# Kernel tuning notes

Measured on AMD Instinct MI355X. Metric: run time of the kernel, lower is better.

Reference implementation:

```python
import jax, jax.numpy as jnp
import numpy as np

N_NODES = 100000
HIDDEN = 128
N_EDGES = 1000000


def setup_inputs() -> dict:
    key = jax.random.key(0)
    k1, k2, k3 = jax.random.split(key, 3)
    z = jax.random.normal(k1, (N_NODES, HIDDEN), dtype=jnp.float32)
    edge_index = jax.random.randint(k2, (2, N_EDGES), 0, N_NODES, dtype=jnp.int64)
    # xavier_uniform for square matrix: bound = sqrt(6/(fan_in+fan_out))
    bound = float(np.sqrt(6.0 / (HIDDEN + HIDDEN)))
    weights = jax.random.uniform(k3, (HIDDEN, HIDDEN), dtype=jnp.float32,
                                 minval=-bound, maxval=bound)
    return {"z": z, "edge_index": edge_index, "weights": weights}


def reference(z, edge_index, weights):
    # symm=True: symmetrize the bilinear form
    W = weights + weights.T                      # [d, d]
    z_src = z[edge_index[0]]                     # [E, d] gather
    z_dst = z[edge_index[1]]                     # [E, d] gather
    # torch: (W @ z_dst.T).T == z_dst @ W.T
    value = jnp.einsum('ed,dk,ek->e', z_src, W, z_dst)  # row-wise bilinear score
    return jax.nn.sigmoid(value)
```

## Files before the change

### kernel.cpp

```cpp
#include <hip/hip_runtime.h>

#define HIDDEN 128
#define SLOT_H 264
#define BSHIFT 10
#define NBMAX 128

typedef _Float16 f16;
typedef f16 f16x2 __attribute__((ext_vector_type(2)));
typedef f16 f16x8 __attribute__((ext_vector_type(8)));
typedef float f32x16 __attribute__((ext_vector_type(16)));
typedef unsigned long long ull;

static __device__ __forceinline__ float fdot2(f16x2 a, f16x2 b, float c) {
    return __builtin_amdgcn_fdot2(a, b, c, false);
}

__global__ __launch_bounds__(256) void prep_w(const float* __restrict__ w,
                                              f16* __restrict__ wsh_t,
                                              int* __restrict__ hist) {
    int idx = blockIdx.x * 256 + threadIdx.x;
    if (idx < 2 * NBMAX) hist[idx] = 0;
    int n = idx >> 7, k = idx & 127;
    wsh_t[idx] = (f16)(w[k * HIDDEN + n] + w[n * HIDDEN + k]);
}

__global__ __launch_bounds__(256) void hist_k(const int* __restrict__ eidx,
                                              int* __restrict__ hist, int E, int nb) {
    __shared__ int h[NBMAX];
    int tid = threadIdx.x;
    if (tid < NBMAX) h[tid] = 0;
    __syncthreads();
    for (int e = blockIdx.x * 256 + tid; e < E; e += gridDim.x * 256)
        atomicAdd(&h[eidx[E + e] >> BSHIFT], 1);
    __syncthreads();
    if (tid < nb && h[tid]) atomicAdd(&hist[tid], h[tid]);
}

__global__ void scan_k(const int* __restrict__ hist, int* __restrict__ cursor, int nb) {
    if (threadIdx.x == 0) {
        int s = 0;
        for (int i = 0; i < nb; ++i) { cursor[i] = s; s += hist[i]; }
    }
}

__global__ __launch_bounds__(256) void scatter_k(const int* __restrict__ eidx,
                                                 int* __restrict__ cursor,
                                                 ull* __restrict__ perm, int E, int nb) {
    __shared__ int lh[NBMAX], lbase[NBMAX], lrank[NBMAX];
    int tid = threadIdx.x;
    int base = blockIdx.x * 4096;
    if (tid < NBMAX) { lh[tid] = 0; lrank[tid] = 0; }
    __syncthreads();
    int s[16], d[16], bb[16];
    #pragma unroll
    for (int i = 0; i < 16; ++i) {
        int e = base + i * 256 + tid;
        bb[i] = -1;
        if (e < E) {
            s[i] = eidx[e]; d[i] = eidx[E + e];
            bb[i] = d[i] >> BSHIFT;
            atomicAdd(&lh[bb[i]], 1);
        }
    }
    __syncthreads();
    if (tid < nb && lh[tid]) lbase[tid] = atomicAdd(&cursor[tid], lh[tid]);
    __syncthreads();
    #pragma unroll
    for (int i = 0; i < 16; ++i) {
        if (bb[i] >= 0) {
            int e = base + i * 256 + tid;
            int r = atomicAdd(&lrank[bb[i]], 1);
            perm[lbase[bb[i]] + r] =
                (ull)s[i] | ((ull)d[i] << 17) | ((ull)e << 34);
        }
    }
}

__global__ __launch_bounds__(256, 3) void gemm_mfma2(const float* __restrict__ z,
                                                     const f16* __restrict__ wsh_t,
                                                     f16* __restrict__ zh,
                                                     f16* __restrict__ uh, int nrows) {
    __shared__ f16 afrag[64 * SLOT_H];
    int tid = threadIdx.x;
    int row0 = blockIdx.x * 128;
    if (row0 > nrows - 128) row0 = nrows - 128;

    {
        const float4* zg = (const float4*)(z + (size_t)row0 * HIDDEN);
        f16x8* zhg = (f16x8*)(zh + (size_t)row0 * HIDDEN);
        #pragma unroll
        for (int it = 0; it < 8; ++it) {
            int g = it * 256 + tid;
            float4 v0 = zg[2 * g];
            float4 v1 = zg[2 * g + 1];
            f16x8 h = {(f16)v0.x, (f16)v0.y, (f16)v0.z, (f16)v0.w,
                       (f16)v1.x, (f16)v1.y, (f16)v1.z, (f16)v1.w};
            zhg[g] = h;
            int row = g >> 4, ch = g & 15;
            int slot = (row >> 5) * 16 + ch;
            *(f16x8*)&afrag[slot * SLOT_H + (row & 31) * 8] = h;
        }
    }
    __syncthreads();

    int wave = tid >> 6, lane = tid & 63;
    int m = lane & 31, half = lane >> 5;
    const f16* wb = wsh_t + (size_t)m * HIDDEN + half * 8;

    f32x16 acc0, acc1, acc2, acc3;
    #pragma unroll
    for (int r = 0; r < 16; ++r) { acc0[r] = 0.f; acc1[r] = 0.f; acc2[r] = 0.f; acc3[r] = 0.f; }

    #pragma unroll
    for (int ks = 0; ks < 8; ++ks) {
        f16x8 a = *(const f16x8*)&afrag[(wave * 16 + ks * 2 + half) * SLOT_H + m * 8];
        f16x8 b0 = *(const f16x8*)&wb[ 0 * HIDDEN + 16 * ks];
        f16x8 b1 = *(const f16x8*)&wb[32 * HIDDEN + 16 * ks];
        f16x8 b2 = *(const f16x8*)&wb[64 * HIDDEN + 16 * ks];
        f16x8 b3 = *(const f16x8*)&wb[96 * HIDDEN + 16 * ks];
        acc0 = __builtin_amdgcn_mfma_f32_32x32x16_f16(a, b0, acc0, 0, 0, 0);
        acc1 = __builtin_amdgcn_mfma_f32_32x32x16_f16(a, b1, acc1, 0, 0, 0);
        acc2 = __builtin_amdgcn_mfma_f32_32x32x16_f16(a, b2, acc2, 0, 0, 0);
        acc3 = __builtin_amdgcn_mfma_f32_32x32x16_f16(a, b3, acc3, 0, 0, 0);
    }

    f16* ur = uh + (size_t)(row0 + wave * 32) * HIDDEN;
    #pragma unroll
    for (int r = 0; r < 16; ++r) {
        int row = (r & 3) + 8 * (r >> 2) + 4 * half;
        f16* p = ur + (size_t)row * HIDDEN + m;
        p[0]  = (f16)acc0[r];
        p[32] = (f16)acc1[r];
        p[64] = (f16)acc2[r];
        p[96] = (f16)acc3[r];
    }
}

__global__ __launch_bounds__(256) void edge_bin(const f16* __restrict__ uh,
                                                const f16* __restrict__ zh,
                                                const ull* __restrict__ perm,
                                                float* __restrict__ out, int E, int cpx) {
    int tid = threadIdx.x;
    int g = tid >> 4, t = tid & 15;
    int b = blockIdx.x;
    int chunk = (b & 7) * cpx + (b >> 3);
    int e = chunk * 16 + g;
    if (e >= E) return;
    ull p = perm[e];
    int src = (int)(p & 0x1FFFF);
    int dst = (int)((p >> 17) & 0x1FFFF);
    int eid = (int)(p >> 34);
    const float4* a4 = (const float4*)(uh + (size_t)src * HIDDEN);
    const float4* b4 = (const float4*)(zh + (size_t)dst * HIDDEN);
    float4 av = a4[t], bv = b4[t];
    const f16x2* ap = (const f16x2*)&av;
    const f16x2* bp = (const f16x2*)&bv;
    float s = 0.f;
    #pragma unroll
    for (int i = 0; i < 4; ++i) s = fdot2(ap[i], bp[i], s);
    #pragma unroll
    for (int off = 8; off > 0; off >>= 1) s += __shfl_down(s, off, 16);
    if (t == 0) out[eid] = 1.0f / (1.0f + __expf(-s));
}

__global__ __launch_bounds__(256) void edge_score16(const f16* __restrict__ uh,
                                                    const f16* __restrict__ zh,
                                                    const int* __restrict__ eidx,
                                                    float* __restrict__ out, int E) {
    int tid = threadIdx.x;
    int g = tid >> 4, t = tid & 15;
    int e = blockIdx.x * 16 + g;
    if (e >= E) return;
    int src = eidx[e];
    int dst = eidx[E + e];
    const float4* a4 = (const float4*)(uh + (size_t)src * HIDDEN);
    const float4* b4 = (const float4*)(zh + (size_t)dst * HIDDEN);
    float4 av = a4[t], bv = b4[t];
    const f16x2* ap = (const f16x2*)&av;
    const f16x2* bp = (const f16x2*)&bv;
    float s = 0.f;
    #pragma unroll
    for (int i = 0; i < 4; ++i) s = fdot2(ap[i], bp[i], s);
    #pragma unroll
    for (int off = 8; off > 0; off >>= 1) s += __shfl_down(s, off, 16);
    if (t == 0) out[e] = 1.0f / (1.0f + __expf(-s));
}

extern "C" void kernel_launch(void* const* d_in, const int* in_sizes, int n_in,
                              void* d_out, int out_size, void* d_ws, size_t ws_size,
                              hipStream_t stream) {
    const float* z    = (const float*)d_in[0];
    const int*   eidx = (const int*)d_in[1];
    const float* w    = (const float*)d_in[2];
    float* out = (float*)d_out;

    int nrows = in_sizes[0] / HIDDEN;
    int E = out_size;
    int nb = (nrows >> BSHIFT) + 1;

    f16* wsh_t = (f16*)d_ws;
    f16* zh    = wsh_t + HIDDEN * HIDDEN;
    f16* uh    = zh + (size_t)nrows * HIDDEN;
    int* hist  = (int*)(uh + (size_t)nrows * HIDDEN);
    int* cursor = hist + NBMAX;
    ull* perm  = (ull*)(cursor + NBMAX);

    size_t need = (size_t)((char*)(perm + E) - (char*)d_ws);
    bool binned = ws_size >= need;

    prep_w<<<64, 256, 0, stream>>>(w, wsh_t, hist);
    if (binned) {
        hist_k<<<256, 256, 0, stream>>>(eidx, hist, E, nb);
        scan_k<<<1, 64, 0, stream>>>(hist, cursor, nb);
        scatter_k<<<(E + 4095) / 4096, 256, 0, stream>>>(eidx, cursor, perm, E, nb);
    }
    gemm_mfma2<<<(nrows + 127) / 128, 256, 0, stream>>>(z, wsh_t, zh, uh, nrows);
    if (binned) {
        int nch = (E + 15) / 16;
        int cpx = (nch + 7) / 8;
        edge_bin<<<8 * cpx, 256, 0, stream>>>(uh, zh, perm, out, E, cpx);
    } else {
        edge_score16<<<(E + 15) / 16, 256, 0, stream>>>(uh, zh, eidx, out, E);
    }
}
```

Measured before the change: 193.6 us.

## Replace histogram+scan binning with fixed-capacity buckets and overflow list

Drops the histogram and serial scan kernels and gives each destination bucket a fixed-capacity slot range, so scatter can start directly from preset cursors. Edges past a bucket's capacity go to an overflow buffer that a separate kernel scores. The edge kernel now launches over all padded slots and skips the empty ones, which adds some idle blocks plus an extra launch. It also switches the uh gather to a nontemporal load. This assumes bucket sizes rarely exceed the capacity. Overflow is capped, and any edges beyond that cap would be silently dropped.

Result: slower. 221.4 us (+14.4%).

```diff
diff --git a/kernel.cpp b/kernel.cpp
--- a/kernel.cpp
+++ b/kernel.cpp
@@ -4,10 +4,13 @@
 #define SLOT_H 264
 #define BSHIFT 10
 #define NBMAX 128
+#define CAP 11264
+#define OVF_MAX 65536
 
 typedef _Float16 f16;
 typedef f16 f16x2 __attribute__((ext_vector_type(2)));
 typedef f16 f16x8 __attribute__((ext_vector_type(8)));
+typedef float f32x4 __attribute__((ext_vector_type(4)));
 typedef float f32x16 __attribute__((ext_vector_type(16)));
 typedef unsigned long long ull;
 
@@ -17,35 +20,21 @@
 
 __global__ __launch_bounds__(256) void prep_w(const float* __restrict__ w,
                                               f16* __restrict__ wsh_t,
-                                              int* __restrict__ hist) {
+                                              int* __restrict__ cursor,
+                                              int* __restrict__ ovf_cnt) {
     int idx = blockIdx.x * 256 + threadIdx.x;
-    if (idx < 2 * NBMAX) hist[idx] = 0;
+    if (idx < NBMAX) cursor[idx] = idx * CAP;
+    if (idx == NBMAX) ovf_cnt[0] = 0;
     int n = idx >> 7, k = idx & 127;
     wsh_t[idx] = (f16)(w[k * HIDDEN + n] + w[n * HIDDEN + k]);
 }
 
-__global__ __launch_bounds__(256) void hist_k(const int* __restrict__ eidx,
-                                              int* __restrict__ hist, int E, int nb) {
-    __shared__ int h[NBMAX];
-    int tid = threadIdx.x;
-    if (tid < NBMAX) h[tid] = 0;
-    __syncthreads();
-    for (int e = blockIdx.x * 256 + tid; e < E; e += gridDim.x * 256)
-        atomicAdd(&h[eidx[E + e] >> BSHIFT], 1);
-    __syncthreads();
-    if (tid < nb && h[tid]) atomicAdd(&hist[tid], h[tid]);
-}
-
-__global__ void scan_k(const int* __restrict__ hist, int* __restrict__ cursor, int nb) {
-    if (threadIdx.x == 0) {
-        int s = 0;
-        for (int i = 0; i < nb; ++i) { cursor[i] = s; s += hist[i]; }
-    }
-}
-
 __global__ __launch_bounds__(256) void scatter_k(const int* __restrict__ eidx,
                                                  int* __restrict__ cursor,
-                                                 ull* __restrict__ perm, int E, int nb) {
+                                                 ull* __restrict__ perm,
+                                                 ull* __restrict__ ovf,
+                                                 int* __restrict__ ovf_cnt,
+                                                 int E, int nb) {
     __shared__ int lh[NBMAX], lbase[NBMAX], lrank[NBMAX];
     int tid = threadIdx.x;
     int base = blockIdx.x * 4096;
@@ -70,8 +59,13 @@
         if (bb[i] >= 0) {
             int e = base + i * 256 + tid;
             int r = atomicAdd(&lrank[bb[i]], 1);
-            perm[lbase[bb[i]] + r] =
-                (ull)s[i] | ((ull)d[i] << 17) | ((ull)e << 34);
+            long pos = (long)lbase[bb[i]] + r;
+            ull v = (ull)s[i] | ((ull)d[i] << 17) | ((ull)e << 34);
+            if (pos < (long)(bb[i] + 1) * CAP) perm[pos] = v;
+            else {
+                int o = atomicAdd(ovf_cnt, 1);
+                if (o < OVF_MAX) ovf[o] = v;
+            }
         }
     }
 }
@@ -136,31 +130,53 @@
     }
 }
 
+static __device__ __forceinline__ void score_edge(const f16* uh, const f16* zh,
+                                                  ull p, float* out, int t) {
+    int src = (int)(p & 0x1FFFF);
+    int dst = (int)((p >> 17) & 0x1FFFF);
+    int eid = (int)(p >> 34);
+    const f32x4* a4 = (const f32x4*)(uh + (size_t)src * HIDDEN);
+    const f32x4* b4 = (const f32x4*)(zh + (size_t)dst * HIDDEN);
+    f32x4 av = __builtin_nontemporal_load(&a4[t]);
+    f32x4 bv = b4[t];
+    const f16x2* ap = (const f16x2*)&av;
+    const f16x2* bp = (const f16x2*)&bv;
+    float s = 0.f;
+    #pragma unroll
+    for (int i = 0; i < 4; ++i) s = fdot2(ap[i], bp[i], s);
+    #pragma unroll
+    for (int off = 8; off > 0; off >>= 1) s += __shfl_down(s, off, 16);
+    if (t == 0) out[eid] = 1.0f / (1.0f + __expf(-s));
+}
+
 __global__ __launch_bounds__(256) void edge_bin(const f16* __restrict__ uh,
                                                 const f16* __restrict__ zh,
                                                 const ull* __restrict__ perm,
-                                                float* __restrict__ out, int E, int cpx) {
+                                                const int* __restrict__ cursor,
+                                                float* __restrict__ out, int cpx) {
     int tid = threadIdx.x;
     int g = tid >> 4, t = tid & 15;
     int b = blockIdx.x;
     int chunk = (b & 7) * cpx + (b >> 3);
-    int e = chunk * 16 + g;
-    if (e >= E) return;
-    ull p = perm[e];
-    int src = (int)(p & 0x1FFFF);
-    int dst = (int)((p >> 17) & 0x1FFFF);
-    int eid = (int)(p >> 34);
-    const float4* a4 = (const float4*)(uh + (size_t)src * HIDDEN);
-    const float4* b4 = (const float4*)(zh + (size_t)dst * HIDDEN);
-    float4 av = a4[t], bv = b4[t];
-    const f16x2* ap = (const f16x2*)&av;
-    const f16x2* bp = (const f16x2*)&bv;
-    float s = 0.f;
-    #pragma unroll
-    for (int i = 0; i < 4; ++i) s = fdot2(ap[i], bp[i], s);
-    #pragma unroll
-    for (int off = 8; off > 0; off >>= 1) s += __shfl_down(s, off, 16);
-    if (t == 0) out[eid] = 1.0f / (1.0f + __expf(-s));
+    long slot = (long)chunk * 16 + g;
+    int bk = (int)(slot / CAP);
+    int end = cursor[bk];
+    int lim = (bk + 1) * CAP;
+    if (slot >= (end < lim ? end : lim)) return;
+    score_edge(uh, zh, perm[slot], out, t);
+}
+
+__global__ __launch_bounds__(256) void edge_ovf(const f16* __restrict__ uh,
+                                                const f16* __restrict__ zh,
+                                                const ull* __restrict__ ovf,
+                                                const int* __restrict__ ovf_cnt,
+                                                float* __restrict__ out) {
+    int n = ovf_cnt[0];
+    if (n > OVF_MAX) n = OVF_MAX;
+    int tid = threadIdx.x;
+    int g = tid >> 4, t = tid & 15;
+    for (int i = blockIdx.x * 16 + g; i < n; i += gridDim.x * 16)
+        score_edge(uh, zh, ovf[i], out, t);
 }
 
 __global__ __launch_bounds__(256) void edge_score16(const f16* __restrict__ uh,
@@ -171,19 +187,8 @@
     int g = tid >> 4, t = tid & 15;
     int e = blockIdx.x * 16 + g;
     if (e >= E) return;
-    int src = eidx[e];
-    int dst = eidx[E + e];
-    const float4* a4 = (const float4*)(uh + (size_t)src * HIDDEN);
-    const float4* b4 = (const float4*)(zh + (size_t)dst * HIDDEN);
-    float4 av = a4[t], bv = b4[t];
-    const f16x2* ap = (const f16x2*)&av;
-    const f16x2* bp = (const f16x2*)&bv;
-    float s = 0.f;
-    #pragma unroll
-    for (int i = 0; i < 4; ++i) s = fdot2(ap[i], bp[i], s);
-    #pragma unroll
-    for (int off = 8; off > 0; off >>= 1) s += __shfl_down(s, off, 16);
-    if (t == 0) out[e] = 1.0f / (1.0f + __expf(-s));
+    ull p = (ull)eidx[e] | ((ull)eidx[E + e] << 17) | ((ull)e << 34);
+    score_edge(uh, zh, p, out, t);
 }
 
 extern "C" void kernel_launch(void* const* d_in, const int* in_sizes, int n_in,
@@ -198,27 +203,27 @@
     int E = out_size;
     int nb = (nrows >> BSHIFT) + 1;
 
-    f16* wsh_t = (f16*)d_ws;
-    f16* zh    = wsh_t + HIDDEN * HIDDEN;
-    f16* uh    = zh + (size_t)nrows * HIDDEN;
-    int* hist  = (int*)(uh + (size_t)nrows * HIDDEN);
-    int* cursor = hist + NBMAX;
-    ull* perm  = (ull*)(cursor + NBMAX);
-
-    size_t need = (size_t)((char*)(perm + E) - (char*)d_ws);
+    f16* wsh_t  = (f16*)d_ws;
+    f16* zh     = wsh_t + HIDDEN * HIDDEN;
+    f16* uh     = zh + (size_t)nrows * HIDDEN;
+    int* cursor = (int*)(uh + (size_t)nrows * HIDDEN);
+    int* ovf_cnt = cursor + NBMAX;
+    ull* ovf    = (ull*)(ovf_cnt + 2);
+    ull* perm   = ovf + OVF_MAX;
+
+    long nslots = (long)nb * CAP;
+    size_t need = (size_t)((char*)(perm + nslots) - (char*)d_ws);
     bool binned = ws_size >= need;
 
-    prep_w<<<64, 256, 0, stream>>>(w, wsh_t, hist);
-    if (binned) {
-        hist_k<<<256, 256, 0, stream>>>(eidx, hist, E, nb);
-        scan_k<<<1, 64, 0, stream>>>(hist, cursor, nb);
-        scatter_k<<<(E + 4095) / 4096, 256, 0, stream>>>(eidx, cursor, perm, E, nb);
-    }
+    prep_w<<<64, 256, 0, stream>>>(w, wsh_t, cursor, ovf_cnt);
+    if (binned)
+        scatter_k<<<(E + 4095) / 4096, 256, 0, stream>>>(eidx, cursor, perm, ovf, ovf_cnt, E, nb);
     gemm_mfma2<<<(nrows + 127) / 128, 256, 0, stream>>>(z, wsh_t, zh, uh, nrows);
     if (binned) {
-        int nch = (E + 15) / 16;
-        int cpx = (nch + 7) / 8;
-        edge_bin<<<8 * cpx, 256, 0, stream>>>(uh, zh, perm, out, E, cpx);
+        long nch = (nslots + 15) / 16;
+        int cpx = (int)((nch + 7) / 8);
+        edge_bin<<<8 * cpx, 256, 0, stream>>>(uh, zh, perm, cursor, out, cpx);
+        edge_ovf<<<32, 256, 0, stream>>>(uh, zh, ovf, ovf_cnt, out);
     } else {
         edge_score16<<<(E + 15) / 16, 256, 0, stream>>>(uh, zh, eidx, out, E);
     }
```
